# Kernel tuning notes

Measured on AMD Instinct MI355X. Metric: run time of the kernel, lower is better.

## Reference

```python
import jax, jax.numpy as jnp
import numpy as np

NPOINT = 1024
RADIUS = 0.2
NSAMPLE = 32


def furthest_point_sampling(xyz, npoint):
    # xyz: (B, N, 3) -> (B, npoint) int32 indices
    B, N, _ = xyz.shape

    def step(carry, _):
        dist, far = carry
        centroid = jnp.take_along_axis(xyz, far[:, None, None], axis=1)  # (B,1,3)
        d = jnp.sum((xyz - centroid) ** 2, axis=-1)                       # (B,N)
        dist = jnp.minimum(dist, d)
        new_far = jnp.argmax(dist, axis=-1).astype(jnp.int32)
        return (dist, new_far), far

    init = (jnp.full((B, N), 1e10, xyz.dtype), jnp.zeros((B,), jnp.int32))
    _, idx = jax.lax.scan(step, init, None, length=npoint)
    return idx.T  # (B, npoint)


def ball_query(xyz, new_xyz, radius, nsample):
    # xyz: (B,N,3), new_xyz: (B,S,3) -> (B,S,nsample) int32 indices
    N = xyz.shape[1]
    d2 = jnp.sum((new_xyz[:, :, None, :] - xyz[:, None, :, :]) ** 2, axis=-1)  # (B,S,N)
    # pick first `nsample` indices within radius (CUDA ball_query semantics)
    key = jnp.where(d2 < radius * radius, jnp.arange(N, dtype=jnp.int32)[None, None, :], N)
    idx = jnp.sort(key, axis=-1)[..., :nsample]          # (B,S,nsample)
    first = idx[..., :1]
    idx = jnp.where(idx == N, first, idx)                # pad with first valid
    return jnp.clip(idx, 0, N - 1).astype(jnp.int32)     # guard empty balls


def sa_forward(xyz, features, W1, s1, b1, W2, s2, b2, W3, s3, b3):
    B, N, _ = xyz.shape
    center_idx = furthest_point_sampling(xyz, NPOINT)                     # (B,S)
    new_xyz = jnp.take_along_axis(xyz, center_idx[..., None], axis=1)     # (B,S,3)

    idx = ball_query(xyz, new_xyz, RADIUS, NSAMPLE)                       # (B,S,K)
    # group xyz (relative coords) and features
    g_xyz = jnp.take_along_axis(xyz[:, None], idx[..., None], axis=2)     # (B,S,K,3)
    g_xyz = g_xyz - new_xyz[:, :, None, :]
    feats_n = jnp.swapaxes(features, 1, 2)                                # (B,N,C)
    g_feat = jnp.take_along_axis(feats_n[:, None], idx[..., None], axis=2)  # (B,S,K,C)
    g = jnp.concatenate([g_xyz, g_feat], axis=-1)                         # (B,S,K,3+C)
    x = jnp.transpose(g, (0, 3, 1, 2))                                    # (B,3+C,S,K)

    # 1x1 conv MLP with (folded) BN affine + ReLU
    for W, s, b in ((W1, s1, b1), (W2, s2, b2), (W3, s3, b3)):
        x = jax.nn.relu(jnp.einsum('oi,bisk->bosk', W, x)
                        * s[None, :, None, None] + b[None, :, None, None])
    new_features = jnp.max(x, axis=-1)                                    # (B,Cout,S)
    return new_xyz, new_features


def setup_inputs() -> dict:
    key = jax.random.key(0)
    ks = jax.random.split(key, 11)
    B, N, C = 4, 16384, 64
    return {
        'xyz': jax.random.uniform(ks[0], (B, N, 3), jnp.float32),
        'features': jax.random.normal(ks[1], (B, C, N), jnp.float32),
        'W1': jax.random.normal(ks[2], (64, C + 3), jnp.float32) * 0.1,
        's1': jax.random.uniform(ks[3], (64,), jnp.float32),
        'b1': jax.random.normal(ks[4], (64,), jnp.float32) * 0.1,
        'W2': jax.random.normal(ks[5], (64, 64), jnp.float32) * 0.1,
        's2': jax.random.uniform(ks[6], (64,), jnp.float32),
        'b2': jax.random.normal(ks[7], (64,), jnp.float32) * 0.1,
        'W3': jax.random.normal(ks[8], (128, 64), jnp.float32) * 0.1,
        's3': jax.random.uniform(ks[9], (128,), jnp.float32),
        'b3': jax.random.normal(ks[10], (128,), jnp.float32) * 0.1,
    }


def reference(xyz, features, W1, s1, b1, W2, s2, b2, W3, s3, b3):
    return sa_forward(xyz, features, W1, s1, b1, W2, s2, b2, W3, s3, b3)
```

## Files before the change

### kernel.cpp

```cpp
#include <hip/hip_runtime.h>
#include <cstdint>
#include <cstddef>

#pragma clang fp contract(off)

#define BATCH   4
#define NPTS    16384
#define NPOINT  1024
#define NSAMPLE 32
#define CIN     67
#define R2f     0.04f

#define FPS_T   512
#define FPS_PAD 34

#define RPT16(M) M(0)M(1)M(2)M(3)M(4)M(5)M(6)M(7)M(8)M(9)M(10)M(11)M(12)M(13)M(14)M(15)

typedef float v2f __attribute__((ext_vector_type(2)));

template <int CTRL, int RMASK>
__device__ __forceinline__ void amax_dpp(float& v, int& i) {
  int nv = __builtin_amdgcn_update_dpp(__float_as_int(v), __float_as_int(v),
                                       CTRL, RMASK, 0xf, false);
  int ni = __builtin_amdgcn_update_dpp(i, i, CTRL, RMASK, 0xf, false);
  float fv = __int_as_float(nv);
  bool tk = (fv > v) || (fv == v && ni < i);
  v = tk ? fv : v;
  i = tk ? ni : i;
}

__global__ void __launch_bounds__(FPS_T)
fps_kernel(const float* __restrict__ xyz, float* __restrict__ out_newxyz)
{
  __shared__ float px[FPS_T * FPS_PAD];
  __shared__ float py[FPS_T * FPS_PAD];
  __shared__ float s_wv[2][8];
  __shared__ int   s_wi[2][8];

  const int b = blockIdx.x;
  const float* base = xyz + (size_t)b * NPTS * 3;
  const int t = threadIdx.x;
  const int lane = t & 63, w = t >> 6;
  const int t34 = t * FPS_PAD;

#define INITP(j) v2f pz##j, dd##j; { \
    const float* p0 = base + (size_t)(((2*(j)) << 9) + t) * 3; \
    const float* p1 = base + (size_t)(((2*(j)+1) << 9) + t) * 3; \
    px[t34 + 2*(j)]     = p0[0];  px[t34 + 2*(j) + 1] = p1[0]; \
    py[t34 + 2*(j)]     = p0[1];  py[t34 + 2*(j) + 1] = p1[1]; \
    pz##j.x = p0[2];  pz##j.y = p1[2]; \
    dd##j.x = 1e10f;  dd##j.y = 1e10f; }
  RPT16(INITP)
#undef INITP

  float cx = base[0], cy = base[1], cz = base[2];

  for (int it = 0; it < NPOINT; ++it) {
#define PINJ(j) asm volatile("" : "+v"(pz##j), "+v"(dd##j));
    RPT16(PINJ)
#undef PINJ

    if (t == 0) {
      int o = (b * NPOINT + it) * 3;
      out_newxyz[o + 0] = cx;
      out_newxyz[o + 1] = cy;
      out_newxyz[o + 2] = cz;
    }

    v2f cx2, cy2, cz2;
    cx2.x = cx; cx2.y = cx;
    cy2.x = cy; cy2.y = cy;
    cz2.x = cz; cz2.y = cz;

    float bv = -1.0f; int bl = 0;
#define STEP2(j) { \
    v2f xx = *reinterpret_cast<const v2f*>(&px[t34 + 2*(j)]); \
    v2f yy = *reinterpret_cast<const v2f*>(&py[t34 + 2*(j)]); \
    v2f dx = xx - cx2; \
    v2f dy = yy - cy2; \
    v2f dz = pz##j - cz2; \
    v2f sx = dx * dx; \
    v2f sy = dy * dy; \
    v2f sz = dz * dz; \
    v2f d2 = (sx + sy) + sz; \
    v2f nd; \
    nd.x = fminf(dd##j.x, d2.x); \
    nd.y = fminf(dd##j.y, d2.y); \
    dd##j = nd; \
    float m = fmaxf(nd.x, nd.y); \
    int kw = (nd.x >= nd.y) ? (2*(j)) : (2*(j)+1);   \
    bool tk = m > bv;                                \
    bv = tk ? m : bv; \
    bl = tk ? kw : bl; }
    RPT16(STEP2)
#undef STEP2
    int bi = (bl << 9) + t;

    amax_dpp<0x121, 0xf>(bv, bi);
    amax_dpp<0x122, 0xf>(bv, bi);
    amax_dpp<0x124, 0xf>(bv, bi);
    amax_dpp<0x128, 0xf>(bv, bi);
    amax_dpp<0x142, 0xa>(bv, bi);
    amax_dpp<0x143, 0xc>(bv, bi);

    const int par = it & 1;
    if (lane == 63) { s_wv[par][w] = bv; s_wi[par][w] = bi; }
    __syncthreads();

    float gv = s_wv[par][lane & 7];
    int   gi = s_wi[par][lane & 7];
    amax_dpp<0x121, 0xf>(gv, gi);
    amax_dpp<0x122, 0xf>(gv, gi);
    amax_dpp<0x124, 0xf>(gv, gi);

    int far = __builtin_amdgcn_readfirstlane(gi);
    cx = base[far * 3 + 0];
    cy = base[far * 3 + 1];
    cz = base[far * 3 + 2];
  }
}

__global__ __launch_bounds__(256) void transpose_kernel(
    const float* __restrict__ f, float* __restrict__ ft)
{
  __shared__ float tile[64][65];
  int b  = blockIdx.x >> 8;
  int n0 = (blockIdx.x & 255) << 6;
  for (int v = threadIdx.x; v < 64 * 64; v += 256) {
    int c = v >> 6, j = v & 63;
    tile[c][j] = f[((size_t)(b * 64 + c)) * NPTS + n0 + j];
  }
  __syncthreads();
  for (int v = threadIdx.x; v < 64 * 64; v += 256) {
    int j = v >> 6, c = v & 63;
    ft[((size_t)(b * NPTS + n0 + j)) * 64 + c] = tile[c][j];
  }
}

__global__ __launch_bounds__(1024) void mlp_kernel(
    const float* __restrict__ xyz,
    const float* __restrict__ feats,
    const float* __restrict__ featsT,
    const float* __restrict__ nx,
    const float* __restrict__ W1, const float* __restrict__ s1, const float* __restrict__ b1,
    const float* __restrict__ W2, const float* __restrict__ s2, const float* __restrict__ b2,
    const float* __restrict__ W3, const float* __restrict__ s3, const float* __restrict__ b3,
    float* __restrict__ outF)
{
  __shared__ float W1t[CIN * 64];
  __shared__ float W2t[64 * 64];
  __shared__ float sb[512];
  __shared__ float xs[CIN * 34];
  __shared__ float h1[64 * 34];
  __shared__ float h2[64 * 34];
  __shared__ int   hm[128];
  __shared__ int   lid8[8][NSAMPLE];

  const int tid = threadIdx.x;
  const int lane = tid & 63, w = tid >> 6;

  for (int v = tid; v < CIN * 64; v += 1024) {
    int o = v / CIN, i = v - o * CIN;
    W1t[i * 64 + o] = W1[v];
  }
  for (int v = tid; v < 64 * 64; v += 1024) {
    int o = v >> 6, i = v & 63;
    W2t[i * 64 + o] = W2[v];
  }
  if (tid < 64)       sb[tid]       = s1[tid];
  else if (tid < 128) sb[tid]       = b1[tid - 64];
  else if (tid < 192) sb[tid]       = s2[tid - 128];
  else if (tid < 256) sb[tid]       = b2[tid - 192];
  else if (tid < 384) sb[tid]       = s3[tid - 256];
  else if (tid < 512) sb[tid]       = b3[tid - 384];

  if (w < 8) {
    int g = (blockIdx.x << 3) + w;
    int b = g >> 10;
    const float* base = xyz + (size_t)b * NPTS * 3;
    float cx = nx[g * 3 + 0], cy = nx[g * 3 + 1], cz = nx[g * 3 + 2];
    int cnt = 0, fidx = -1;
    for (int c0 = 0; c0 < NPTS && cnt < NSAMPLE; c0 += 64) {
      int i = c0 + lane;
      float dx = __fsub_rn(base[i * 3 + 0], cx);
      float dy = __fsub_rn(base[i * 3 + 1], cy);
      float dz = __fsub_rn(base[i * 3 + 2], cz);
      float d2 = __fadd_rn(__fadd_rn(__fmul_rn(dx, dx), __fmul_rn(dy, dy)),
                           __fmul_rn(dz, dz));
      bool pred = d2 < R2f;
      unsigned long long mk = __ballot(pred);
      if (pred) {
        int rank = cnt + __popcll(mk & ((1ull << lane) - 1ull));
        if (rank < NSAMPLE) lid8[w][rank] = i;
        if (rank == 0) fidx = i;
      }
      cnt += __popcll(mk);
    }
#pragma unroll
    for (int off = 32; off >= 1; off >>= 1) {
      int o = __shfl_xor(fidx, off);
      fidx = o > fidx ? o : fidx;
    }
    if (lane >= cnt && lane < NSAMPLE) lid8[w][lane] = fidx;
  }
  __syncthreads();

  for (int ci = 0; ci < 8; ++ci) {
    int g = (blockIdx.x << 3) + ci;
    int b = g >> 10, m = g & 1023;

    {
      int k = tid >> 5, c0 = tid & 31;
      int id = lid8[ci][k];
      for (int c = c0; c < CIN; c += 32) {
        float val;
        if (c < 3)
          val = __fsub_rn(xyz[((size_t)b * NPTS + id) * 3 + c], nx[g * 3 + c]);
        else if (featsT)
          val = featsT[((size_t)b * NPTS + id) * 64 + (c - 3)];
        else
          val = feats[((size_t)(b * 64 + (c - 3))) * NPTS + id];
        xs[c * 34 + k] = val;
      }
      if (tid < 128) hm[tid] = 0;
    }
    __syncthreads();

    {
      int oc = tid & 63, k0 = (tid >> 6) << 1;
      float a0 = 0.f, a1 = 0.f;
#pragma unroll 4
      for (int i = 0; i < CIN; ++i) {
        float ww = W1t[i * 64 + oc];
        a0 = fmaf(ww, xs[i * 34 + k0], a0);
        a1 = fmaf(ww, xs[i * 34 + k0 + 1], a1);
      }
      float s = sb[oc], bb = sb[64 + oc];
      h1[oc * 34 + k0]     = fmaxf(fmaf(a0, s, bb), 0.f);
      h1[oc * 34 + k0 + 1] = fmaxf(fmaf(a1, s, bb), 0.f);
    }
    __syncthreads();

    {
      int oc = tid & 63, k0 = (tid >> 6) << 1;
      float a0 = 0.f, a1 = 0.f;
#pragma unroll 4
      for (int i = 0; i < 64; ++i) {
        float ww = W2t[i * 64 + oc];
        a0 = fmaf(ww, h1[i * 34 + k0], a0);
        a1 = fmaf(ww, h1[i * 34 + k0 + 1], a1);
      }
      float s = sb[128 + oc], bb = sb[192 + oc];
      h2[oc * 34 + k0]     = fmaxf(fmaf(a0, s, bb), 0.f);
      h2[oc * 34 + k0 + 1] = fmaxf(fmaf(a1, s, bb), 0.f);
    }
    __syncthreads();

    {
      int oc = tid & 127, k0 = (tid >> 7) << 2;
      const float4* W3v = reinterpret_cast<const float4*>(W3);
      float a0 = 0.f, a1 = 0.f, a2 = 0.f, a3 = 0.f;
#pragma unroll 4
      for (int i4 = 0; i4 < 16; ++i4) {
        float4 wv = W3v[oc * 16 + i4];
        const float* hr = &h2[(i4 * 4) * 34 + k0];
        a0 = fmaf(wv.x, hr[0], a0); a1 = fmaf(wv.x, hr[1], a1);
        a2 = fmaf(wv.x, hr[2], a2); a3 = fmaf(wv.x, hr[3], a3);
        hr += 34;
        a0 = fmaf(wv.y, hr[0], a0); a1 = fmaf(wv.y, hr[1], a1);
        a2 = fmaf(wv.y, hr[2], a2); a3 = fmaf(wv.y, hr[3], a3);
        hr += 34;
        a0 = fmaf(wv.z, hr[0], a0); a1 = fmaf(wv.z, hr[1], a1);
        a2 = fmaf(wv.z, hr[2], a2); a3 = fmaf(wv.z, hr[3], a3);
        hr += 34;
        a0 = fmaf(wv.w, hr[0], a0); a1 = fmaf(wv.w, hr[1], a1);
        a2 = fmaf(wv.w, hr[2], a2); a3 = fmaf(wv.w, hr[3], a3);
      }
      float s = sb[256 + oc], bb = sb[384 + oc];
      float v0 = fmaxf(fmaf(a0, s, bb), 0.f);
      float v1 = fmaxf(fmaf(a1, s, bb), 0.f);
      float v2 = fmaxf(fmaf(a2, s, bb), 0.f);
      float v3 = fmaxf(fmaf(a3, s, bb), 0.f);
      float mv = fmaxf(fmaxf(v0, v1), fmaxf(v2, v3));
      atomicMax(&hm[oc], __float_as_int(mv));
    }
    __syncthreads();

    if (tid < 128)
      outF[(((size_t)b * 128 + tid) << 10) + m] = __int_as_float(hm[tid]);
    __syncthreads();
  }
}

extern "C" void kernel_launch(void* const* d_in, const int* in_sizes, int n_in,
                              void* d_out, int out_size, void* d_ws, size_t ws_size,
                              hipStream_t stream)
{
  if (n_in < 11) return;
  const float* xyz   = (const float*)d_in[0];
  const float* feats = (const float*)d_in[1];
  const float* W1 = (const float*)d_in[2];
  const float* s1 = (const float*)d_in[3];
  const float* b1 = (const float*)d_in[4];
  const float* W2 = (const float*)d_in[5];
  const float* s2 = (const float*)d_in[6];
  const float* b2 = (const float*)d_in[7];
  const float* W3 = (const float*)d_in[8];
  const float* s3 = (const float*)d_in[9];
  const float* b3 = (const float*)d_in[10];
  float* out = (float*)d_out;

  float* featsT = nullptr;
  size_t needT = (size_t)BATCH * NPTS * 64 * sizeof(float);
  if (ws_size >= needT) featsT = (float*)d_ws;

  fps_kernel<<<BATCH, FPS_T, 0, stream>>>(xyz, out);
  if (featsT) transpose_kernel<<<BATCH * 256, 256, 0, stream>>>(feats, featsT);
  mlp_kernel<<<512, 1024, 0, stream>>>(xyz, feats, featsT, out,
                                       W1, s1, b1, W2, s2, b2, W3, s3, b3,
                                       out + BATCH * NPOINT * 3);
}
```

Baseline: 2.283 ms.

## Add spatial-grid FPS that skips cells whose bounding box cannot update

```diff
diff --git a/kernel.cpp b/kernel.cpp
--- a/kernel.cpp
+++ b/kernel.cpp
@@ -12,6 +12,7 @@
 #define R2f     0.04f
 
 #define FPS_T   512
+#define NCELL   512
 #define FPS_PAD 34
 
 #define RPT16(M) M(0)M(1)M(2)M(3)M(4)M(5)M(6)M(7)M(8)M(9)M(10)M(11)M(12)M(13)M(14)M(15)
@@ -29,8 +30,171 @@
   i = tk ? ni : i;
 }
 
+__device__ __forceinline__ unsigned f2o(float f) {
+  unsigned u = __float_as_uint(f);
+  return u ^ ((unsigned)((int)u >> 31) | 0x80000000u);
+}
+__device__ __forceinline__ float o2f(unsigned k) {
+  unsigned u = (k & 0x80000000u) ? (k ^ 0x80000000u) : ~k;
+  return __uint_as_float(u);
+}
+
 __global__ void __launch_bounds__(FPS_T)
-fps_kernel(const float* __restrict__ xyz, float* __restrict__ out_newxyz)
+fps_grid(const float* __restrict__ xyz, float* __restrict__ out_newxyz,
+         float4* __restrict__ ws)
+{
+  __shared__ float    dd[NPTS];
+  __shared__ int      cnt[NCELL];
+  __shared__ int      cstart[NCELL];
+  __shared__ int      ccur[NCELL];
+  __shared__ unsigned abx[NCELL], aby[NCELL], abz[NCELL];
+  __shared__ unsigned aBx[NCELL], aBy[NCELL], aBz[NCELL];
+  __shared__ float    s_wv[2][8];
+  __shared__ int      s_wi[2][8];
+
+  const int b = blockIdx.x;
+  const float* base = xyz + (size_t)b * NPTS * 3;
+  float4* sp = ws + (size_t)b * NPTS;
+  const int t = threadIdx.x;
+  const int lane = t & 63, w = t >> 6;
+
+  cnt[t] = 0;
+  abx[t] = 0xFFFFFFFFu; aby[t] = 0xFFFFFFFFu; abz[t] = 0xFFFFFFFFu;
+  aBx[t] = 0u;          aBy[t] = 0u;          aBz[t] = 0u;
+  __syncthreads();
+
+  for (int k = 0; k < 32; ++k) {
+    int idx = (k << 9) + t;
+    const float* p = base + (size_t)idx * 3;
+    float x = p[0], y = p[1], z = p[2];
+    int ix = (int)(x * 8.0f); ix = ix < 0 ? 0 : (ix > 7 ? 7 : ix);
+    int iy = (int)(y * 8.0f); iy = iy < 0 ? 0 : (iy > 7 ? 7 : iy);
+    int iz = (int)(z * 8.0f); iz = iz < 0 ? 0 : (iz > 7 ? 7 : iz);
+    int ci = ix | (iy << 3) | (iz << 6);
+    atomicAdd(&cnt[ci], 1);
+    atomicMin(&abx[ci], f2o(x)); atomicMax(&aBx[ci], f2o(x));
+    atomicMin(&aby[ci], f2o(y)); atomicMax(&aBy[ci], f2o(y));
+    atomicMin(&abz[ci], f2o(z)); atomicMax(&aBz[ci], f2o(z));
+  }
+  __syncthreads();
+
+  if (w == 0) {
+    int loc[8]; int s = 0;
+#pragma unroll
+    for (int i = 0; i < 8; ++i) { loc[i] = s; s += cnt[lane * 8 + i]; }
+    int run = s;
+#pragma unroll
+    for (int off = 1; off < 64; off <<= 1) {
+      int o = __shfl_up(run, off);
+      if (lane >= off) run += o;
+    }
+    int excl = run - s;
+#pragma unroll
+    for (int i = 0; i < 8; ++i) cstart[lane * 8 + i] = excl + loc[i];
+  }
+  __syncthreads();
+  ccur[t] = cstart[t];
+  __syncthreads();
+
+  for (int k = 0; k < 32; ++k) {
+    int idx = (k << 9) + t;
+    const float* p = base + (size_t)idx * 3;
+    float x = p[0], y = p[1], z = p[2];
+    int ix = (int)(x * 8.0f); ix = ix < 0 ? 0 : (ix > 7 ? 7 : ix);
+    int iy = (int)(y * 8.0f); iy = iy < 0 ? 0 : (iy > 7 ? 7 : iy);
+    int iz = (int)(z * 8.0f); iz = iz < 0 ? 0 : (iz > 7 ? 7 : iz);
+    int ci = ix | (iy << 3) | (iz << 6);
+    int pos = atomicAdd(&ccur[ci], 1);
+    sp[pos] = make_float4(x, y, z, __int_as_float(idx));
+    dd[pos] = 1e10f;
+  }
+  __threadfence_block();
+  __syncthreads();
+
+  const int mystart = cstart[t], mycnt = cnt[t];
+  float bxlo, bylo, bzlo, bxhi, byhi, bzhi;
+  if (mycnt > 0) {
+    bxlo = o2f(abx[t]); bxhi = o2f(aBx[t]);
+    bylo = o2f(aby[t]); byhi = o2f(aBy[t]);
+    bzlo = o2f(abz[t]); bzhi = o2f(aBz[t]);
+  } else {
+    bxlo = bxhi = bylo = byhi = bzlo = bzhi = 1e3f;
+  }
+  float cmax = (mycnt > 0) ? 1e10f : -1.0f;
+  int   cargi = 0;
+
+  const float4* cp = sp + mystart;
+  float* dp = dd + mystart;
+
+  float cx = base[0], cy = base[1], cz = base[2];
+
+  for (int it = 0; it < NPOINT; ++it) {
+    if (t == 0) {
+      int o = (b * NPOINT + it) * 3;
+      out_newxyz[o + 0] = cx;
+      out_newxyz[o + 1] = cy;
+      out_newxyz[o + 2] = cz;
+    }
+
+    float qx = fminf(fmaxf(cx, bxlo), bxhi);
+    float qy = fminf(fmaxf(cy, bylo), byhi);
+    float qz = fminf(fmaxf(cz, bzlo), bzhi);
+    float ex = cx - qx, ey = cy - qy, ez = cz - qz;
+    float lb2 = (ex * ex + ey * ey) + ez * ez;
+
+    if (!(lb2 > cmax + 1e-5f)) {
+      float m = -1.0f; int mi = 0;
+#define UPD(Q, E, PI) { \
+      float dx = (Q).x - cx, dy = (Q).y - cy, dz = (Q).z - cz; \
+      float d2 = (dx * dx + dy * dy) + dz * dz; \
+      float nd = fminf((E), d2); \
+      dp[PI] = nd; \
+      int qi = __float_as_int((Q).w); \
+      bool tk = (nd > m) || (nd == m && qi < mi); \
+      m = tk ? nd : m; \
+      mi = tk ? qi : mi; }
+      int p = 0;
+      for (; p + 4 <= mycnt; p += 4) {
+        float4 q0 = cp[p], q1 = cp[p + 1], q2 = cp[p + 2], q3 = cp[p + 3];
+        float  e0 = dp[p], e1 = dp[p + 1], e2 = dp[p + 2], e3 = dp[p + 3];
+        UPD(q0, e0, p); UPD(q1, e1, p + 1); UPD(q2, e2, p + 2); UPD(q3, e3, p + 3);
+      }
+      for (; p < mycnt; ++p) {
+        float4 q = cp[p]; float e = dp[p];
+        UPD(q, e, p);
+      }
+#undef UPD
+      cmax = m; cargi = mi;
+    }
+
+    float bv = cmax; int bi = cargi;
+
+    amax_dpp<0x121, 0xf>(bv, bi);
+    amax_dpp<0x122, 0xf>(bv, bi);
+    amax_dpp<0x124, 0xf>(bv, bi);
+    amax_dpp<0x128, 0xf>(bv, bi);
+    amax_dpp<0x142, 0xa>(bv, bi);
+    amax_dpp<0x143, 0xc>(bv, bi);
+
+    const int par = it & 1;
+    if (lane == 63) { s_wv[par][w] = bv; s_wi[par][w] = bi; }
+    __syncthreads();
+
+    float gv = s_wv[par][lane & 7];
+    int   gi = s_wi[par][lane & 7];
+    amax_dpp<0x121, 0xf>(gv, gi);
+    amax_dpp<0x122, 0xf>(gv, gi);
+    amax_dpp<0x124, 0xf>(gv, gi);
+
+    int far = __builtin_amdgcn_readfirstlane(gi);
+    cx = base[far * 3 + 0];
+    cy = base[far * 3 + 1];
+    cz = base[far * 3 + 2];
+  }
+}
+
+__global__ void __launch_bounds__(FPS_T)
+fps_single(const float* __restrict__ xyz, float* __restrict__ out_newxyz)
 {
   __shared__ float px[FPS_T * FPS_PAD];
   __shared__ float py[FPS_T * FPS_PAD];
@@ -59,19 +223,14 @@
 #define PINJ(j) asm volatile("" : "+v"(pz##j), "+v"(dd##j));
     RPT16(PINJ)
 #undef PINJ
-
     if (t == 0) {
       int o = (b * NPOINT + it) * 3;
       out_newxyz[o + 0] = cx;
       out_newxyz[o + 1] = cy;
       out_newxyz[o + 2] = cz;
     }
-
     v2f cx2, cy2, cz2;
-    cx2.x = cx; cx2.y = cx;
-    cy2.x = cy; cy2.y = cy;
-    cz2.x = cz; cz2.y = cz;
-
+    cx2.x = cx; cx2.y = cx; cy2.x = cy; cy2.y = cy; cz2.x = cz; cz2.y = cz;
     float bv = -1.0f; int bl = 0;
 #define STEP2(j) { \
     v2f xx = *reinterpret_cast<const v2f*>(&px[t34 + 2*(j)]); \
@@ -79,17 +238,14 @@
     v2f dx = xx - cx2; \
     v2f dy = yy - cy2; \
     v2f dz = pz##j - cz2; \
-    v2f sx = dx * dx; \
-    v2f sy = dy * dy; \
-    v2f sz = dz * dz; \
-    v2f d2 = (sx + sy) + sz; \
+    v2f d2 = (dx * dx + dy * dy) + dz * dz; \
     v2f nd; \
     nd.x = fminf(dd##j.x, d2.x); \
     nd.y = fminf(dd##j.y, d2.y); \
     dd##j = nd; \
     float m = fmaxf(nd.x, nd.y); \
-    int kw = (nd.x >= nd.y) ? (2*(j)) : (2*(j)+1);   \
-    bool tk = m > bv;                                \
+    int kw = (nd.x >= nd.y) ? (2*(j)) : (2*(j)+1); \
+    bool tk = m > bv; \
     bv = tk ? m : bv; \
     bl = tk ? kw : bl; }
     RPT16(STEP2)
@@ -310,11 +466,17 @@
   const float* b3 = (const float*)d_in[10];
   float* out = (float*)d_out;
 
+  size_t gridBytes = (size_t)BATCH * NPTS * sizeof(float4);
+  size_t needT = (size_t)BATCH * NPTS * 64 * sizeof(float);
   float* featsT = nullptr;
-  size_t needT = (size_t)BATCH * NPTS * 64 * sizeof(float);
-  if (ws_size >= needT) featsT = (float*)d_ws;
-
-  fps_kernel<<<BATCH, FPS_T, 0, stream>>>(xyz, out);
+  if (ws_size >= gridBytes + needT)
+    featsT = (float*)((char*)d_ws + gridBytes);
+
+  if (ws_size >= gridBytes)
+    fps_grid<<<BATCH, FPS_T, 0, stream>>>(xyz, out, (float4*)d_ws);
+  else
+    fps_single<<<BATCH, FPS_T, 0, stream>>>(xyz, out);
+
   if (featsT) transpose_kernel<<<BATCH * 256, 256, 0, stream>>>(feats, featsT);
   mlp_kernel<<<512, 1024, 0, stream>>>(xyz, feats, featsT, out,
                                        W1, s1, b1, W2, s2, b2, W3, s3, b3,
```

Result: slower. 5.780 ms (+153.2%).
